# Performance work log

Hardware: AMD Instinct MI355X
Metric: run time of the kernel (lower is better)

The kernel has to match this reference:

```python
import jax, jax.numpy as jnp
import numpy as np

E, H, F = 1024, 16, 4096
WH, WW = 32, 32
B = 4
L = WH * WW           # 1024 cross-attn kv tokens
N = L + 1             # 1025 decoder tokens (CLS + window)
D = E // H
SCALE = D ** -0.5
NEG = -1e9            # stands in for -inf in the causal mask


def _rel_coords(Wh, Ww):
    coords = np.stack(np.meshgrid(np.arange(Wh), np.arange(Ww), indexing='ij')).reshape(2, -1)
    rc = (coords[:, :, None] - coords[:, None, :]).transpose(1, 2, 0).astype(np.int64)
    rc[:, :, 0] += Wh - 1
    rc[:, :, 1] += Ww - 1
    rc[:, :, 0] *= 2 * Ww - 1
    return rc.sum(-1)  # (L, L)


def rel_index_self(Wh, Ww):
    nrd = (2 * Wh - 1) * (2 * Ww - 1) + 3
    l = Wh * Ww
    idx = np.zeros((l + 1, l + 1), dtype=np.int32)
    idx[1:, 1:] = _rel_coords(Wh, Ww)
    idx[0, :] = nrd - 3
    idx[:, 0] = nrd - 2
    idx[0, 0] = nrd - 1
    return idx


def rel_index_cross(Wh, Ww):
    nrd = (2 * Wh - 1) * (2 * Ww - 1) + 1
    l = Wh * Ww
    idx = np.zeros((l + 1, l), dtype=np.int32)
    idx[1:, :] = _rel_coords(Wh, Ww)
    idx[0, :] = nrd - 1
    return idx


IDX_SELF = jnp.asarray(rel_index_self(WH, WW))    # (N, N) int32
IDX_CROSS = jnp.asarray(rel_index_cross(WH, WW))  # (N, L) int32
CAUSAL = jnp.triu(jnp.full((N, N), NEG, jnp.float32), 1)


def _ln(x, g, b, eps=1e-5):
    m = x.mean(-1, keepdims=True)
    v = ((x - m) ** 2).mean(-1, keepdims=True)
    return (x - m) * jax.lax.rsqrt(v + eps) * g + b


def setup_inputs():
    key = jax.random.key(0)
    ks = jax.random.split(key, 24)
    g = lambda i, shape, s=0.02: jax.random.normal(ks[i], shape, jnp.float32) * s
    return dict(
        x=g(0, (B, N, E), 1.0),
        y=g(1, (B, L, E), 1.0),
        norm1_g=jnp.ones((E,), jnp.float32), norm1_b=jnp.zeros((E,), jnp.float32),
        norm2_g=jnp.ones((E,), jnp.float32), norm2_b=jnp.zeros((E,), jnp.float32),
        norm3_g=jnp.ones((E,), jnp.float32), norm3_b=jnp.zeros((E,), jnp.float32),
        sa_qkv_w=g(2, (3 * E, E)),
        sa_q_bias=g(3, (E,)),
        sa_v_bias=g(4, (E,)),
        sa_rpb=g(5, ((2 * WH - 1) * (2 * WW - 1) + 3, H)),
        sa_proj_w=g(6, (E, E)), sa_proj_b=g(7, (E,)),
        ca_q_w=g(8, (E, E)),
        ca_kv_w=g(9, (2 * E, E)),
        ca_q_bias=g(10, (E,)),
        ca_v_bias=g(11, (E,)),
        ca_rpb=g(12, ((2 * WH - 1) * (2 * WW - 1) + 1, H)),
        ca_proj_w=g(13, (E, E)), ca_proj_b=g(14, (E,)),
        fc1_w=g(15, (F, E)), fc1_b=g(16, (F,)),
        fc2_w=g(17, (E, F)), fc2_b=g(18, (E,)),
        gamma1=jnp.full((E,), 0.1, jnp.float32),
        gamma2=jnp.full((E,), 0.1, jnp.float32),
        gamma3=jnp.full((E,), 0.1, jnp.float32),
    )


def reference(x, y, norm1_g, norm1_b, norm2_g, norm2_b, norm3_g, norm3_b,
              sa_qkv_w, sa_q_bias, sa_v_bias, sa_rpb, sa_proj_w, sa_proj_b,
              ca_q_w, ca_kv_w, ca_q_bias, ca_v_bias, ca_rpb, ca_proj_w, ca_proj_b,
              fc1_w, fc1_b, fc2_w, fc2_b, gamma1, gamma2, gamma3):
    # cross_attn.extract_kv(y): k gets zero bias, v gets v_bias
    kv_bias = jnp.concatenate([jnp.zeros((E,), x.dtype), ca_v_bias])
    kv = (y @ ca_kv_w.T + kv_bias).reshape(B, L, 2, H, D)
    ck = kv[:, :, 0].transpose(0, 2, 1, 3)  # (B,H,L,D)
    cv = kv[:, :, 1].transpose(0, 2, 1, 3)

    # --- causal self-attention with gathered relative-position bias ---
    h = _ln(x, norm1_g, norm1_b)
    qkv_bias = jnp.concatenate([sa_q_bias, jnp.zeros((E,), x.dtype), sa_v_bias])
    qkv = (h @ sa_qkv_w.T + qkv_bias).reshape(B, N, 3, H, D)
    q = qkv[:, :, 0].transpose(0, 2, 1, 3) * SCALE  # (B,H,N,D)
    k = qkv[:, :, 1].transpose(0, 2, 1, 3)
    v = qkv[:, :, 2].transpose(0, 2, 1, 3)
    bias = sa_rpb[IDX_SELF].transpose(2, 0, 1) + CAUSAL  # (H,N,N)
    attn = jnp.einsum('bhqd,bhkd->bhqk', q, k) + bias[None]
    attn = jax.nn.softmax(attn, axis=-1)
    sa = jnp.einsum('bhqk,bhkd->bhqd', attn, v).transpose(0, 2, 1, 3).reshape(B, N, E)
    sa = sa @ sa_proj_w.T + sa_proj_b
    x = x + gamma1 * sa

    # --- cross-attention with gathered relative-position bias ---
    h = _ln(x, norm2_g, norm2_b)
    q = (h @ ca_q_w.T + ca_q_bias).reshape(B, N, H, D).transpose(0, 2, 1, 3) * SCALE
    cbias = ca_rpb[IDX_CROSS].transpose(2, 0, 1)  # (H,N,L)
    attn = jnp.einsum('bhqd,bhkd->bhqk', q, ck) + cbias[None]
    attn = jax.nn.softmax(attn, axis=-1)
    ca = jnp.einsum('bhqk,bhkd->bhqd', attn, cv).transpose(0, 2, 1, 3).reshape(B, N, E)
    ca = ca @ ca_proj_w.T + ca_proj_b
    x = x + gamma2 * ca

    # --- FFN (Linear -> GELU -> Linear, no inner identity) ---
    h = _ln(x, norm3_g, norm3_b)
    h = jax.nn.gelu(h @ fc1_w.T + fc1_b, approximate=False)
    h = h @ fc2_w.T + fc2_b
    x = x + gamma3 * h
    return x
```

## Files before the change

### kernel.cpp

```cpp
#include <hip/hip_runtime.h>
#include <hip/hip_bf16.h>
#include <math.h>

typedef __bf16 bf16;
typedef __bf16 bf16x8 __attribute__((ext_vector_type(8)));
typedef float f32x4 __attribute__((ext_vector_type(4)));

#define MP    4224
#define MACT  4100
#define NQTOK 1025
#define NKTOK 1024
#define EDIM  1024
#define FDIM  4096
#define NHEAD 16
#define HD    64
#define QSCALE 0.125f
#define VTS   1056

__device__ __forceinline__ void glds16(const bf16* g, bf16* l) {
  __builtin_amdgcn_global_load_lds(
      (const __attribute__((address_space(1))) void*)g,
      (__attribute__((address_space(3))) void*)l, 16, 0, 0);
}

__device__ __forceinline__ bf16x8 ld8(const void* p, size_t i, bool f32) {
  if (f32) {
    const float* q = (const float*)p + i;
    bf16x8 r;
#pragma unroll
    for (int j = 0; j < 8; ++j) r[j] = (bf16)q[j];
    return r;
  }
  return *(const bf16x8*)((const bf16*)p + i);
}

struct WPtrs { const float* s[8]; };
__global__ __launch_bounds__(256) void conv_kernel(WPtrs wp, bf16* dst) {
  const size_t sz[8] = {3145728UL, 1048576UL, 1048576UL, 2097152UL,
                        1048576UL, 4194304UL, 4194304UL, 4194304UL};
  size_t id = ((size_t)blockIdx.x * 256 + threadIdx.x) * 8;
  size_t off = 0;
#pragma unroll
  for (int i = 0; i < 8; ++i) {
    if (id < off + sz[i]) {
      const float* s = wp.s[i] + (id - off);
      bf16x8 r;
#pragma unroll
      for (int j = 0; j < 8; ++j) r[j] = (bf16)s[j];
      *(bf16x8*)(dst + id) = r;
      return;
    }
    off += sz[i];
  }
}

__global__ void zero_pads_kernel(bf16* hln) {
  int i = blockIdx.x * 256 + threadIdx.x;
  const int n = (MP - MACT) * EDIM;
  if (i < n) hln[(size_t)MACT * EDIM + i] = (bf16)0.0f;
}

template<bool FIRST>
__global__ __launch_bounds__(256) void ln_kernel(const float* __restrict__ src,
    float* __restrict__ xf, bf16* __restrict__ out,
    const float* __restrict__ g, const float* __restrict__ bta) {
  const int row = blockIdx.x;
  const int tid = threadIdx.x;
  float v[4];
#pragma unroll
  for (int i = 0; i < 4; ++i) {
    v[i] = src[(size_t)row * EDIM + tid + i * 256];
    if (FIRST) xf[(size_t)row * EDIM + tid + i * 256] = v[i];
  }
  float s = 0.f, sq = 0.f;
#pragma unroll
  for (int i = 0; i < 4; ++i) { s += v[i]; sq += v[i] * v[i]; }
#pragma unroll
  for (int m = 32; m >= 1; m >>= 1) {
    s += __shfl_xor(s, m);
    sq += __shfl_xor(sq, m);
  }
  __shared__ float ss[4], ssq[4];
  const int wave = tid >> 6;
  if ((tid & 63) == 0) { ss[wave] = s; ssq[wave] = sq; }
  __syncthreads();
  s = ss[0] + ss[1] + ss[2] + ss[3];
  sq = ssq[0] + ssq[1] + ssq[2] + ssq[3];
  const float mean = s * (1.f / EDIM);
  const float var = sq * (1.f / EDIM) - mean * mean;
  const float rstd = rsqrtf(var + 1e-5f);
#pragma unroll
  for (int i = 0; i < 4; ++i) {
    int e = tid + i * 256;
    out[(size_t)row * EDIM + e] = (bf16)((v[i] - mean) * rstd * g[e] + bta[e]);
  }
}

enum { EPI_QKV = 0, EPI_KV = 1, EPI_Q = 2, EPI_RES = 3, EPI_GELU = 4, EPI_FINAL = 5 };

template<int EPI, bool ASY>
__global__ __launch_bounds__(256) void gemm_bt(
    const void* __restrict__ A, const void* __restrict__ Bw,
    int K, int Kc,
    const float* __restrict__ bias0, const float* __restrict__ bias1,
    const float* __restrict__ gamma, float* __restrict__ xf,
    bf16* __restrict__ out0, bf16* __restrict__ out1, bf16* __restrict__ out2,
    float* __restrict__ outf)
{
  constexpr int LDP = ASY ? 32 : 40;
  __shared__ bf16 As[128][LDP];
  __shared__ bf16 Bs[128][LDP];
  const int tid = threadIdx.x;
  const int lane = tid & 63, wave = tid >> 6;
  const int quad = lane >> 4, l16 = lane & 15;
  const int wr = wave >> 1, wc = wave & 1;
  const int m0 = blockIdx.y * 128, n0 = blockIdx.x * 128;
  const int kbase = blockIdx.z * Kc;
  const bool first = (blockIdx.z == 0);
  const int r0 = tid >> 2, c0 = (tid & 3) * 8;

  const bf16* gA = nullptr; const bf16* gB = nullptr;
  bf16* lA = nullptr; bf16* lB = nullptr;
  if (ASY) {
    gA = (const bf16*)A + (size_t)(m0 + wave * 16 + (lane >> 2)) * K + kbase + (lane & 3) * 8;
    gB = (const bf16*)Bw + (size_t)(n0 + wave * 16 + (lane >> 2)) * K + kbase + (lane & 3) * 8;
    lA = &As[wave * 16][0];
    lB = &Bs[wave * 16][0];
  }

  f32x4 acc[4][4];
#pragma unroll
  for (int i = 0; i < 4; ++i)
#pragma unroll
    for (int j = 0; j < 4; ++j)
#pragma unroll
      for (int r = 0; r < 4; ++r) acc[i][j][r] = 0.f;

  for (int k0 = 0; k0 < Kc; k0 += 32) {
    if (ASY) {
      glds16(gA, lA);
      glds16(gA + (size_t)64 * K, lA + 64 * 32);
      glds16(gB, lB);
      glds16(gB + (size_t)64 * K, lB + 64 * 32);
      gA += 32; gB += 32;
    } else {
      const bool f32a = (EPI == EPI_KV);
      const size_t kk = (size_t)(kbase + k0);
      *(bf16x8*)(&As[r0][c0])      = ld8(A,  (size_t)(m0 + r0) * K + kk + c0, f32a);
      *(bf16x8*)(&As[r0 + 64][c0]) = ld8(A,  (size_t)(m0 + r0 + 64) * K + kk + c0, f32a);
      *(bf16x8*)(&Bs[r0][c0])      = ld8(Bw, (size_t)(n0 + r0) * K + kk + c0, true);
      *(bf16x8*)(&Bs[r0 + 64][c0]) = ld8(Bw, (size_t)(n0 + r0 + 64) * K + kk + c0, true);
    }
    __syncthreads();
    bf16x8 af[4], bfv[4];
#pragma unroll
    for (int i = 0; i < 4; ++i) {
      af[i]  = *(const bf16x8*)(&As[wr * 64 + i * 16 + l16][quad * 8]);
      bfv[i] = *(const bf16x8*)(&Bs[wc * 64 + i * 16 + l16][quad * 8]);
    }
#pragma unroll
    for (int mb = 0; mb < 4; ++mb)
#pragma unroll
      for (int nb = 0; nb < 4; ++nb)
        acc[mb][nb] = __builtin_amdgcn_mfma_f32_16x16x32_bf16(af[mb], bfv[nb], acc[mb][nb], 0, 0, 0);
    __syncthreads();
  }

#pragma unroll
  for (int mb = 0; mb < 4; ++mb) {
#pragma unroll
    for (int r = 0; r < 4; ++r) {
      const int gm = m0 + wr * 64 + mb * 16 + quad * 4 + r;
#pragma unroll
      for (int nb = 0; nb < 4; ++nb) {
        const int gn = n0 + wc * 64 + nb * 16 + l16;
        float v = acc[mb][nb][r];
        if (EPI == EPI_QKV) {
          if (gm < MACT) {
            unsigned b = (unsigned)gm / 1025u;
            unsigned t = (unsigned)gm - b * 1025u;
            int sec = gn >> 10, e = gn & 1023;
            int h = e >> 6, d = e & 63;
            if (sec == 0)
              out0[((size_t)(b * NHEAD + h) * NQTOK + t) * HD + d] =
                  (bf16)((v + bias0[e]) * QSCALE);
            else if (sec == 1)
              out1[((size_t)(b * NHEAD + h) * NQTOK + t) * HD + d] = (bf16)v;
            else
              out2[((size_t)(b * NHEAD + h) * HD + d) * VTS + t] =
                  (bf16)(v + bias1[e]);
          }
        } else if (EPI == EPI_KV) {
          unsigned b = (unsigned)gm >> 10;
          unsigned t = (unsigned)gm & 1023u;
          int sec = gn >> 10, e = gn & 1023;
          int h = e >> 6, d = e & 63;
          if (sec == 0)
            out0[((size_t)(b * NHEAD + h) * NKTOK + t) * HD + d] = (bf16)v;
          else
            out1[((size_t)(b * NHEAD + h) * HD + d) * NKTOK + t] =
                (bf16)(v + bias1[e]);
        } else if (EPI == EPI_Q) {
          if (gm < MACT) {
            unsigned b = (unsigned)gm / 1025u;
            unsigned t = (unsigned)gm - b * 1025u;
            int h = gn >> 6, d = gn & 63;
            float add = (v + (first ? bias0[gn] : 0.f)) * QSCALE;
            atomicAdd(&outf[((size_t)(b * NHEAD + h) * NQTOK + t) * HD + d], add);
          }
        } else if (EPI == EPI_RES) {
          if (gm < MACT) {
            float add = gamma[gn] * (v + (first ? bias0[gn] : 0.f));
            atomicAdd(&xf[(size_t)gm * EDIM + gn], add);
          }
        } else if (EPI == EPI_GELU) {
          float z = v + bias0[gn];
          float ge = 0.5f * z * (1.0f + erff(z * 0.70710678118f));
          out0[(size_t)gm * FDIM + gn] = (bf16)ge;
        } else {
          if (gm < MACT) {
            size_t o = (size_t)gm * EDIM + gn;
            float add = gamma[gn] * (v + (first ? bias0[gn] : 0.f));
            if (first) add += xf[o];
            atomicAdd(&outf[o], add);
          }
        }
      }
    }
  }
}

template<bool CROSS>
__global__ __launch_bounds__(256) void attn_kernel(
    const void* __restrict__ Q, const bf16* __restrict__ Kg,
    const bf16* __restrict__ Vg, const float* __restrict__ rpb,
    bf16* __restrict__ out)
{
  const int NK  = CROSS ? NKTOK : NQTOK;
  const int NRD = CROSS ? 3970 : 3972;
  const int VS  = CROSS ? NKTOK : VTS;
  const int qt  = CROSS ? blockIdx.x : (16 - blockIdx.x);
  const int h = blockIdx.y, b = blockIdx.z;
  const int tid = threadIdx.x;
  const int lane = tid & 63, wave = tid >> 6;
  const int quad = lane >> 4, l16 = lane & 15;

  __shared__ bf16 rpb_s[4096];
  __shared__ bf16 Ks[64][72];
  __shared__ bf16 Vt[64][72];
  __shared__ bf16 Ps[4][16][72];

  for (int i = tid; i < 4096; i += 256)
    rpb_s[i] = (bf16)((i < NRD) ? rpb[(size_t)i * NHEAD + h] : 0.f);

  const int q0 = qt * 64;
  const int qrow = q0 + wave * 16 + l16;
  const size_t qhb = (size_t)(b * NHEAD + h) * NQTOK;
  bf16x8 qf0, qf1;
  if (qrow < NQTOK) {
    if (CROSS) {
      const float* Qf = (const float*)Q + (qhb + qrow) * HD;
#pragma unroll
      for (int j = 0; j < 8; ++j) {
        qf0[j] = (bf16)Qf[quad * 8 + j];
        qf1[j] = (bf16)Qf[32 + quad * 8 + j];
      }
    } else {
      const bf16* Qb = (const bf16*)Q;
      qf0 = *(const bf16x8*)(Qb + (qhb + qrow) * HD + quad * 8);
      qf1 = *(const bf16x8*)(Qb + (qhb + qrow) * HD + 32 + quad * 8);
    }
  } else {
#pragma unroll
    for (int j = 0; j < 8; ++j) { qf0[j] = (bf16)0.f; qf1[j] = (bf16)0.f; }
  }

  int qgv[4], qcode[4];
#pragma unroll
  for (int r = 0; r < 4; ++r) {
    int qg = q0 + wave * 16 + quad * 4 + r;
    qgv[r] = qg;
    int p = qg - 1;
    qcode[r] = (qg > 0) ? ((p >> 5) * 63 + (p & 31) + 1984) : 0;
  }

  float m_run[4], l_run[4];
  f32x4 oacc[4];
#pragma unroll
  for (int r = 0; r < 4; ++r) { m_run[r] = -1e30f; l_run[r] = 0.f; }
#pragma unroll
  for (int d = 0; d < 4; ++d)
#pragma unroll
    for (int r = 0; r < 4; ++r) oacc[d][r] = 0.f;

  const size_t kvbK = (size_t)(b * NHEAD + h) * NK;
  const size_t vbase = (size_t)(b * NHEAD + h) * HD;
  const int nch = CROSS ? (NKTOK / 64) : (qt + 1);

  const int rr = tid >> 3;
  const int co = (tid & 7) * 8;

  bf16x8 krg[2], vrg[2];
  auto stage_load = [&](int c) {
    const int kc = c * 64;
#pragma unroll
    for (int vv = 0; vv < 2; ++vv) {
      const int row = rr + vv * 32;
      if (!CROSS && kc + row >= NK) {
#pragma unroll
        for (int j = 0; j < 8; ++j) krg[vv][j] = (bf16)0.f;
      } else {
        krg[vv] = *(const bf16x8*)(Kg + (kvbK + kc + row) * HD + co);
      }
      if (!CROSS && kc + co >= NK) {
#pragma unroll
        for (int j = 0; j < 8; ++j) vrg[vv][j] = (bf16)0.f;
      } else {
        vrg[vv] = *(const bf16x8*)(Vg + (vbase + row) * VS + kc + co);
      }
    }
  };

  stage_load(0);
  for (int c = 0; c < nch; ++c) {
    const int kc = c * 64;
    if (c) __syncthreads();
#pragma unroll
    for (int vv = 0; vv < 2; ++vv) {
      const int row = rr + vv * 32;
      *(bf16x8*)(&Ks[row][co]) = krg[vv];
      *(bf16x8*)(&Vt[row][co]) = vrg[vv];
    }
    __syncthreads();
    if (c + 1 < nch) stage_load(c + 1);

    float sv[4][4];
#pragma unroll
    for (int kb = 0; kb < 4; ++kb) {
      f32x4 a;
#pragma unroll
      for (int r = 0; r < 4; ++r) a[r] = 0.f;
      bf16x8 kf0 = *(const bf16x8*)(&Ks[kb * 16 + l16][quad * 8]);
      bf16x8 kf1 = *(const bf16x8*)(&Ks[kb * 16 + l16][32 + quad * 8]);
      a = __builtin_amdgcn_mfma_f32_16x16x32_bf16(qf0, kf0, a, 0, 0, 0);
      a = __builtin_amdgcn_mfma_f32_16x16x32_bf16(qf1, kf1, a, 0, 0, 0);
      const int kg = kc + kb * 16 + l16;
      int kcode;
      if (CROSS) kcode = (kg >> 5) * 63 + (kg & 31);
      else {
        int k1 = kg - 1;
        kcode = (kg > 0) ? ((k1 >> 5) * 63 + (k1 & 31)) : 0;
      }
#pragma unroll
      for (int r = 0; r < 4; ++r) {
        const int qg = qgv[r];
        bool valid = (kg < NK) && (CROSS || kg <= qg);
        int idx;
        if (CROSS) {
          idx = (qg == 0) ? 3969 : (qcode[r] - kcode);
        } else {
          idx = (qg == 0) ? ((kg == 0) ? 3971 : 3969)
                          : ((kg == 0) ? 3970 : (qcode[r] - kcode));
        }
        sv[kb][r] = valid ? (a[r] + (float)rpb_s[idx]) : -1e30f;
      }
    }

#pragma unroll
    for (int r = 0; r < 4; ++r) {
      float mx = fmaxf(fmaxf(sv[0][r], sv[1][r]), fmaxf(sv[2][r], sv[3][r]));
#pragma unroll
      for (int mk = 8; mk >= 1; mk >>= 1) mx = fmaxf(mx, __shfl_xor(mx, mk));
      const float mnew = fmaxf(m_run[r], mx);
      const float alpha = __expf(m_run[r] - mnew);
      m_run[r] = mnew;
      float rs = 0.f;
#pragma unroll
      for (int kb = 0; kb < 4; ++kb) {
        float p = __expf(sv[kb][r] - mnew);
        rs += p;
        Ps[wave][quad * 4 + r][kb * 16 + l16] = (bf16)p;
      }
#pragma unroll
      for (int mk = 8; mk >= 1; mk >>= 1) rs += __shfl_xor(rs, mk);
      l_run[r] = l_run[r] * alpha + rs;
#pragma unroll
      for (int d = 0; d < 4; ++d) oacc[d][r] *= alpha;
    }

    bf16x8 pf0 = *(const bf16x8*)(&Ps[wave][l16][quad * 8]);
    bf16x8 pf1 = *(const bf16x8*)(&Ps[wave][l16][32 + quad * 8]);
#pragma unroll
    for (int db = 0; db < 4; ++db) {
      bf16x8 vf0 = *(const bf16x8*)(&Vt[db * 16 + l16][quad * 8]);
      bf16x8 vf1 = *(const bf16x8*)(&Vt[db * 16 + l16][32 + quad * 8]);
      oacc[db] = __builtin_amdgcn_mfma_f32_16x16x32_bf16(pf0, vf0, oacc[db], 0, 0, 0);
      oacc[db] = __builtin_amdgcn_mfma_f32_16x16x32_bf16(pf1, vf1, oacc[db], 0, 0, 0);
    }
  }

#pragma unroll
  for (int r = 0; r < 4; ++r) {
    const int qg = qgv[r];
    if (qg < NQTOK) {
      const float inv = 1.f / l_run[r];
      const size_t row = (size_t)b * NQTOK + qg;
#pragma unroll
      for (int db = 0; db < 4; ++db)
        out[row * EDIM + h * HD + db * 16 + l16] = (bf16)(oacc[db][r] * inv);
    }
  }
}

extern "C" void kernel_launch(void* const* d_in, const int* in_sizes, int n_in,
                              void* d_out, int out_size, void* d_ws, size_t ws_size,
                              hipStream_t stream) {
  (void)in_sizes; (void)n_in; (void)out_size;
  const float* x        = (const float*)d_in[0];
  const float* y        = (const float*)d_in[1];
  const float* n1g      = (const float*)d_in[2];
  const float* n1b      = (const float*)d_in[3];
  const float* n2g      = (const float*)d_in[4];
  const float* n2b      = (const float*)d_in[5];
  const float* n3g      = (const float*)d_in[6];
  const float* n3b      = (const float*)d_in[7];
  const float* sa_qkv_w = (const float*)d_in[8];
  const float* sa_qb    = (const float*)d_in[9];
  const float* sa_vb    = (const float*)d_in[10];
  const float* sa_rpb   = (const float*)d_in[11];
  const float* sa_pw    = (const float*)d_in[12];
  const float* sa_pb    = (const float*)d_in[13];
  const float* ca_qw    = (const float*)d_in[14];
  const float* ca_kvw   = (const float*)d_in[15];
  const float* ca_qb    = (const float*)d_in[16];
  const float* ca_vb    = (const float*)d_in[17];
  const float* ca_rpb   = (const float*)d_in[18];
  const float* ca_pw    = (const float*)d_in[19];
  const float* ca_pb    = (const float*)d_in[20];
  const float* fc1_w    = (const float*)d_in[21];
  const float* fc1_b    = (const float*)d_in[22];
  const float* fc2_w    = (const float*)d_in[23];
  const float* fc2_b    = (const float*)d_in[24];
  const float* g1       = (const float*)d_in[25];
  const float* g2       = (const float*)d_in[26];
  const float* g3       = (const float*)d_in[27];
  float* outf = (float*)d_out;
  float* qtf  = (float*)d_out;

  char* w = (char*)d_ws;
  float* xf = (float*)w;  w += (size_t)MP * EDIM * 4;
  bf16* hln = (bf16*)w;   w += (size_t)MP * EDIM * 2;
  char* big = w;          w += (size_t)MP * FDIM * 2;
  const size_t qkv_sz = (size_t)4 * NHEAD * NQTOK * HD * 2;
  bf16* qt = (bf16*)big;
  bf16* kt = (bf16*)(big + qkv_sz);
  bf16* vt = (bf16*)(big + 2 * qkv_sz);
  bf16* h1 = (bf16*)big;
  bf16* wpool = (bf16*)w; w += 20971520UL * 2;
  const bool asy = ((size_t)(w - (char*)d_ws) <= ws_size);

  bf16* qkvw_b = wpool;
  bf16* pw_b   = qkvw_b + 3145728UL;
  bf16* cqw_b  = pw_b   + 1048576UL;
  bf16* ckvw_b = cqw_b  + 1048576UL;
  bf16* cpw_b  = ckvw_b + 2097152UL;
  bf16* fc1w_b = cpw_b  + 1048576UL;
  bf16* fc2w_b = fc1w_b + 4194304UL;
  bf16* y_b    = fc2w_b + 4194304UL;

  if (asy) {
    WPtrs wp = {{sa_qkv_w, sa_pw, ca_qw, ca_kvw, ca_pw, fc1_w, fc2_w, y}};
    conv_kernel<<<10240, 256, 0, stream>>>(wp, wpool);
  }
  zero_pads_kernel<<<dim3(((MP - MACT) * EDIM + 255) / 256), 256, 0, stream>>>(hln);
  hipMemsetAsync(qtf, 0, (size_t)MACT * EDIM * 4, stream);

  ln_kernel<true><<<MACT, 256, 0, stream>>>(x, xf, hln, n1g, n1b);
  if (asy) gemm_bt<EPI_QKV, true><<<dim3(24, 33, 1), 256, 0, stream>>>(hln, qkvw_b, 1024, 1024,
      sa_qb, sa_vb, nullptr, nullptr, qt, kt, vt, nullptr);
  else     gemm_bt<EPI_QKV, false><<<dim3(24, 33, 1), 256, 0, stream>>>(hln, sa_qkv_w, 1024, 1024,
      sa_qb, sa_vb, nullptr, nullptr, qt, kt, vt, nullptr);
  attn_kernel<false><<<dim3(17, NHEAD, 4), 256, 0, stream>>>(qt, kt, vt, sa_rpb, hln);
  if (asy) gemm_bt<EPI_RES, true><<<dim3(8, 33, 2), 256, 0, stream>>>(hln, pw_b, 1024, 512,
      sa_pb, nullptr, g1, xf, nullptr, nullptr, nullptr, nullptr);
  else     gemm_bt<EPI_RES, false><<<dim3(8, 33, 2), 256, 0, stream>>>(hln, sa_pw, 1024, 512,
      sa_pb, nullptr, g1, xf, nullptr, nullptr, nullptr, nullptr);

  ln_kernel<false><<<MACT, 256, 0, stream>>>(xf, nullptr, hln, n2g, n2b);
  if (asy) gemm_bt<EPI_Q, true><<<dim3(8, 33, 2), 256, 0, stream>>>(hln, cqw_b, 1024, 512,
      ca_qb, nullptr, nullptr, nullptr, nullptr, nullptr, nullptr, qtf);
  else     gemm_bt<EPI_Q, false><<<dim3(8, 33, 2), 256, 0, stream>>>(hln, ca_qw, 1024, 512,
      ca_qb, nullptr, nullptr, nullptr, nullptr, nullptr, nullptr, qtf);
  if (asy) gemm_bt<EPI_KV, true><<<dim3(16, 32, 1), 256, 0, stream>>>(y_b, ckvw_b, 1024, 1024,
      nullptr, ca_vb, nullptr, nullptr, kt, vt, nullptr, nullptr);
  else     gemm_bt<EPI_KV, false><<<dim3(16, 32, 1), 256, 0, stream>>>(y, ca_kvw, 1024, 1024,
      nullptr, ca_vb, nullptr, nullptr, kt, vt, nullptr, nullptr);
  attn_kernel<true><<<dim3(17, NHEAD, 4), 256, 0, stream>>>(qtf, kt, vt, ca_rpb, hln);
  if (asy) gemm_bt<EPI_RES, true><<<dim3(8, 33, 2), 256, 0, stream>>>(hln, cpw_b, 1024, 512,
      ca_pb, nullptr, g2, xf, nullptr, nullptr, nullptr, nullptr);
  else     gemm_bt<EPI_RES, false><<<dim3(8, 33, 2), 256, 0, stream>>>(hln, ca_pw, 1024, 512,
      ca_pb, nullptr, g2, xf, nullptr, nullptr, nullptr, nullptr);

  ln_kernel<false><<<MACT, 256, 0, stream>>>(xf, nullptr, hln, n3g, n3b);
  if (asy) gemm_bt<EPI_GELU, true><<<dim3(32, 33, 1), 256, 0, stream>>>(hln, fc1w_b, 1024, 1024,
      fc1_b, nullptr, nullptr, nullptr, h1, nullptr, nullptr, nullptr);
  else     gemm_bt<EPI_GELU, false><<<dim3(32, 33, 1), 256, 0, stream>>>(hln, fc1_w, 1024, 1024,
      fc1_b, nullptr, nullptr, nullptr, h1, nullptr, nullptr, nullptr);
  hipMemsetAsync(outf, 0, (size_t)MACT * EDIM * 4, stream);
  if (asy) gemm_bt<EPI_FINAL, true><<<dim3(8, 33, 4), 256, 0, stream>>>(h1, fc2w_b, 4096, 1024,
      fc2_b, nullptr, g3, xf, nullptr, nullptr, nullptr, outf);
  else     gemm_bt<EPI_FINAL, false><<<dim3(8, 33, 4), 256, 0, stream>>>(h1, fc2_w, 4096, 1024,
      fc2_b, nullptr, g3, xf, nullptr, nullptr, nullptr, outf);
}
```

Before: 826.5 us.

## Replace atomic split-K with direct stores and a separate FC2 partial-sum reduction

Result: faster. 746.7 us (-9.7%).

```diff
diff --git a/kernel.cpp b/kernel.cpp
--- a/kernel.cpp
+++ b/kernel.cpp
@@ -96,7 +96,25 @@
   }
 }
 
-enum { EPI_QKV = 0, EPI_KV = 1, EPI_Q = 2, EPI_RES = 3, EPI_GELU = 4, EPI_FINAL = 5 };
+__global__ __launch_bounds__(256) void fc2_reduce_kernel(
+    const float* __restrict__ p0, const float* __restrict__ xf,
+    const float* __restrict__ bias, const float* __restrict__ gamma,
+    float* __restrict__ outf) {
+  size_t i = ((size_t)blockIdx.x * 256 + threadIdx.x) * 4;
+  if (i >= (size_t)MACT * EDIM) return;
+  f32x4 a = *(const f32x4*)(p0 + i);
+  f32x4 b = *(const f32x4*)(outf + i);
+  f32x4 x = *(const f32x4*)(xf + i);
+  const int gn = (int)(i & (EDIM - 1));
+  f32x4 r;
+#pragma unroll
+  for (int j = 0; j < 4; ++j)
+    r[j] = x[j] + gamma[gn + j] * (a[j] + b[j] + bias[gn + j]);
+  *(f32x4*)(outf + i) = r;
+}
+
+enum { EPI_QKV = 0, EPI_KV = 1, EPI_Q = 2, EPI_RES = 3, EPI_GELU = 4,
+       EPI_FINAL = 5, EPI_PART = 6 };
 
 template<int EPI, bool ASY>
 __global__ __launch_bounds__(256) void gemm_bt(
@@ -205,18 +223,23 @@
             unsigned b = (unsigned)gm / 1025u;
             unsigned t = (unsigned)gm - b * 1025u;
             int h = gn >> 6, d = gn & 63;
-            float add = (v + (first ? bias0[gn] : 0.f)) * QSCALE;
-            atomicAdd(&outf[((size_t)(b * NHEAD + h) * NQTOK + t) * HD + d], add);
+            outf[((size_t)(b * NHEAD + h) * NQTOK + t) * HD + d] =
+                (v + bias0[gn]) * QSCALE;
           }
         } else if (EPI == EPI_RES) {
           if (gm < MACT) {
-            float add = gamma[gn] * (v + (first ? bias0[gn] : 0.f));
-            atomicAdd(&xf[(size_t)gm * EDIM + gn], add);
+            size_t o = (size_t)gm * EDIM + gn;
+            xf[o] += gamma[gn] * (v + bias0[gn]);
           }
         } else if (EPI == EPI_GELU) {
           float z = v + bias0[gn];
           float ge = 0.5f * z * (1.0f + erff(z * 0.70710678118f));
           out0[(size_t)gm * FDIM + gn] = (bf16)ge;
+        } else if (EPI == EPI_PART) {
+          if (gm < MACT) {
+            float* dst = first ? xf : outf;
+            dst[(size_t)gm * EDIM + gn] = v;
+          }
         } else {
           if (gm < MACT) {
             size_t o = (size_t)gm * EDIM + gn;
@@ -467,13 +490,13 @@
   bf16* fc1w_b = cpw_b  + 1048576UL;
   bf16* fc2w_b = fc1w_b + 4194304UL;
   bf16* y_b    = fc2w_b + 4194304UL;
+  float* part0 = (float*)wpool;
 
   if (asy) {
     WPtrs wp = {{sa_qkv_w, sa_pw, ca_qw, ca_kvw, ca_pw, fc1_w, fc2_w, y}};
     conv_kernel<<<10240, 256, 0, stream>>>(wp, wpool);
   }
   zero_pads_kernel<<<dim3(((MP - MACT) * EDIM + 255) / 256), 256, 0, stream>>>(hln);
-  hipMemsetAsync(qtf, 0, (size_t)MACT * EDIM * 4, stream);
 
   ln_kernel<true><<<MACT, 256, 0, stream>>>(x, xf, hln, n1g, n1b);
   if (asy) gemm_bt<EPI_QKV, true><<<dim3(24, 33, 1), 256, 0, stream>>>(hln, qkvw_b, 1024, 1024,
@@ -481,24 +504,24 @@
   else     gemm_bt<EPI_QKV, false><<<dim3(24, 33, 1), 256, 0, stream>>>(hln, sa_qkv_w, 1024, 1024,
       sa_qb, sa_vb, nullptr, nullptr, qt, kt, vt, nullptr);
   attn_kernel<false><<<dim3(17, NHEAD, 4), 256, 0, stream>>>(qt, kt, vt, sa_rpb, hln);
-  if (asy) gemm_bt<EPI_RES, true><<<dim3(8, 33, 2), 256, 0, stream>>>(hln, pw_b, 1024, 512,
+  if (asy) gemm_bt<EPI_RES, true><<<dim3(8, 33, 1), 256, 0, stream>>>(hln, pw_b, 1024, 1024,
       sa_pb, nullptr, g1, xf, nullptr, nullptr, nullptr, nullptr);
-  else     gemm_bt<EPI_RES, false><<<dim3(8, 33, 2), 256, 0, stream>>>(hln, sa_pw, 1024, 512,
+  else     gemm_bt<EPI_RES, false><<<dim3(8, 33, 1), 256, 0, stream>>>(hln, sa_pw, 1024, 1024,
       sa_pb, nullptr, g1, xf, nullptr, nullptr, nullptr, nullptr);
 
   ln_kernel<false><<<MACT, 256, 0, stream>>>(xf, nullptr, hln, n2g, n2b);
-  if (asy) gemm_bt<EPI_Q, true><<<dim3(8, 33, 2), 256, 0, stream>>>(hln, cqw_b, 1024, 512,
+  if (asy) gemm_bt<EPI_Q, true><<<dim3(8, 33, 1), 256, 0, stream>>>(hln, cqw_b, 1024, 1024,
       ca_qb, nullptr, nullptr, nullptr, nullptr, nullptr, nullptr, qtf);
-  else     gemm_bt<EPI_Q, false><<<dim3(8, 33, 2), 256, 0, stream>>>(hln, ca_qw, 1024, 512,
+  else     gemm_bt<EPI_Q, false><<<dim3(8, 33, 1), 256, 0, stream>>>(hln, ca_qw, 1024, 1024,
       ca_qb, nullptr, nullptr, nullptr, nullptr, nullptr, nullptr, qtf);
   if (asy) gemm_bt<EPI_KV, true><<<dim3(16, 32, 1), 256, 0, stream>>>(y_b, ckvw_b, 1024, 1024,
       nullptr, ca_vb, nullptr, nullptr, kt, vt, nullptr, nullptr);
   else     gemm_bt<EPI_KV, false><<<dim3(16, 32, 1), 256, 0, stream>>>(y, ca_kvw, 1024, 1024,
       nullptr, ca_vb, nullptr, nullptr, kt, vt, nullptr, nullptr);
   attn_kernel<true><<<dim3(17, NHEAD, 4), 256, 0, stream>>>(qtf, kt, vt, ca_rpb, hln);
-  if (asy) gemm_bt<EPI_RES, true><<<dim3(8, 33, 2), 256, 0, stream>>>(hln, cpw_b, 1024, 512,
+  if (asy) gemm_bt<EPI_RES, true><<<dim3(8, 33, 1), 256, 0, stream>>>(hln, cpw_b, 1024, 1024,
       ca_pb, nullptr, g2, xf, nullptr, nullptr, nullptr, nullptr);
-  else     gemm_bt<EPI_RES, false><<<dim3(8, 33, 2), 256, 0, stream>>>(hln, ca_pw, 1024, 512,
+  else     gemm_bt<EPI_RES, false><<<dim3(8, 33, 1), 256, 0, stream>>>(hln, ca_pw, 1024, 1024,
       ca_pb, nullptr, g2, xf, nullptr, nullptr, nullptr, nullptr);
 
   ln_kernel<false><<<MACT, 256, 0, stream>>>(xf, nullptr, hln, n3g, n3b);
@@ -506,9 +529,13 @@
       fc1_b, nullptr, nullptr, nullptr, h1, nullptr, nullptr, nullptr);
   else     gemm_bt<EPI_GELU, false><<<dim3(32, 33, 1), 256, 0, stream>>>(hln, fc1_w, 1024, 1024,
       fc1_b, nullptr, nullptr, nullptr, h1, nullptr, nullptr, nullptr);
-  hipMemsetAsync(outf, 0, (size_t)MACT * EDIM * 4, stream);
-  if (asy) gemm_bt<EPI_FINAL, true><<<dim3(8, 33, 4), 256, 0, stream>>>(h1, fc2w_b, 4096, 1024,
-      fc2_b, nullptr, g3, xf, nullptr, nullptr, nullptr, outf);
-  else     gemm_bt<EPI_FINAL, false><<<dim3(8, 33, 4), 256, 0, stream>>>(h1, fc2_w, 4096, 1024,
-      fc2_b, nullptr, g3, xf, nullptr, nullptr, nullptr, outf);
-}
+  if (asy) {
+    gemm_bt<EPI_PART, true><<<dim3(8, 33, 2), 256, 0, stream>>>(h1, fc2w_b, 4096, 2048,
+        nullptr, nullptr, nullptr, part0, nullptr, nullptr, nullptr, outf);
+    fc2_reduce_kernel<<<dim3(4100), 256, 0, stream>>>(part0, xf, fc2_b, g3, outf);
+  } else {
+    hipMemsetAsync(outf, 0, (size_t)MACT * EDIM * 4, stream);
+    gemm_bt<EPI_FINAL, false><<<dim3(8, 33, 4), 256, 0, stream>>>(h1, fc2_w, 4096, 1024,
+        fc2_b, nullptr, g3, xf, nullptr, nullptr, nullptr, outf);
+  }
+}
```
